# Kernel tuning notes

Hardware: AMD Instinct MI355X
Metric: run time of the kernel (lower is better)

## Reference

```python
import jax, jax.numpy as jnp
import numpy as np
from jax import lax

DG = 8  # deformable groups


def conv3(x, w, b):
    # 3x3 stride-1 SAME conv, NCHW/OIHW
    y = lax.conv_general_dilated(x, w, (1, 1), 'SAME',
                                 dimension_numbers=('NCHW', 'OIHW', 'NCHW'))
    return y + b[None, :, None, None]


def lrelu(x):
    return jnp.where(x >= 0, x, 0.1 * x)


def _mdcn(x, offset, mask, w, b, dg):
    """Modulated deformable conv v2: 3x3, stride 1, pad 1, dilation 1, groups 1.
    offset: [B, 2*dg*9, H, W] (first dg*9 = y offsets, second dg*9 = x offsets),
    mask:   [B, dg*9, H, W] (already sigmoided)."""
    B, C, H, W = x.shape
    kk = 9
    Cg = C // dg
    off = offset.reshape(B, 2, dg, kk, H, W)
    oy, ox = off[:, 0], off[:, 1]            # [B, dg, kk, H, W]
    m = mask.reshape(B, dg, kk, H, W)
    ky = (jnp.arange(kk) // 3 - 1).astype(x.dtype).reshape(1, 1, kk, 1, 1)
    kx = (jnp.arange(kk) % 3 - 1).astype(x.dtype).reshape(1, 1, kk, 1, 1)
    hg = jnp.arange(H, dtype=x.dtype).reshape(1, 1, 1, H, 1)
    wg = jnp.arange(W, dtype=x.dtype).reshape(1, 1, 1, 1, W)
    py = hg + ky + oy                        # sampling positions (pad=1 cancels k-1 shift)
    px = wg + kx + ox
    y0 = jnp.floor(py)
    x0 = jnp.floor(px)
    wy = py - y0
    wx = px - x0
    xg = x.reshape(B, dg, Cg, H * W)
    acc = jnp.zeros((B, dg, Cg, kk, H, W), x.dtype)
    for dy, dx, wgt in ((0.0, 0.0, (1 - wy) * (1 - wx)),
                        (0.0, 1.0, (1 - wy) * wx),
                        (1.0, 0.0, wy * (1 - wx)),
                        (1.0, 1.0, wy * wx)):
        yy = y0 + dy
        xx = x0 + dx
        valid = (yy >= 0) & (yy < H) & (xx >= 0) & (xx < W)
        yi = jnp.clip(yy, 0, H - 1).astype(jnp.int32)
        xi = jnp.clip(xx, 0, W - 1).astype(jnp.int32)
        idx = (yi * W + xi).reshape(B, dg, 1, kk * H * W)
        v = jnp.take_along_axis(xg, idx, axis=3).reshape(B, dg, Cg, kk, H, W)
        acc = acc + v * (wgt * valid.astype(x.dtype))[:, :, None]
    acc = acc * m[:, :, None]                # modulation mask
    sampled = acc.reshape(B, C, kk, H, W)
    out = jnp.einsum('bckhw,ock->bohw', sampled, w.reshape(w.shape[0], C, kk))
    return out + b[None, :, None, None]


def _dcn_pack(x, feat, w_om, b_om, w, b):
    out = conv3(feat, w_om, b_om)            # [B, 3*dg*9, H, W]
    o1, o2, mr = jnp.split(out, 3, axis=1)
    offset = jnp.concatenate([o1, o2], axis=1)
    mask = jax.nn.sigmoid(mr)
    return _mdcn(x, offset, mask, w, b, DG)


def _forward(ref, neb,
             w_oc1, b_oc1, w_om1, b_om1, w_dcn1, b_dcn1, w_fc, b_fc,
             w_cas1, b_cas1, w_cas2, b_cas2, w_om2, b_om2, w_dcn2, b_dcn2,
             w_ta1, b_ta1, w_ta2, b_ta2, w_ff, b_ff):
    start = ref
    # --- PCD alignment (nbr_feat_l = neb, ref_feat_l = ref) ---
    off = lrelu(conv3(jnp.concatenate([neb, ref], axis=1), w_oc1, b_oc1))
    feat = _dcn_pack(neb, off, w_om1, b_om1, w_dcn1, b_dcn1)
    feat = lrelu(conv3(feat, w_fc, b_fc))
    off = jnp.concatenate([feat, ref], axis=1)
    off = lrelu(conv3(lrelu(conv3(off, w_cas1, b_cas1)), w_cas2, b_cas2))
    feat = lrelu(_dcn_pack(feat, off, w_om2, b_om2, w_dcn2, b_dcn2))
    # --- TSA fusion (ref=ref, neb=feat) ---
    emb_ref = conv3(ref, w_ta1, b_ta1)
    emb = conv3(feat, w_ta2, b_ta2)
    corr = jnp.sum(emb * emb_ref, axis=1, keepdims=True)  # [B,1,H,W]
    feat = lrelu(conv3(ref * corr, w_ff, b_ff))
    return feat + start


def setup_inputs() -> dict:
    key = jax.random.key(0)
    ks = jax.random.split(key, 32)
    B, C, H, W = 4, 64, 180, 320
    s = 0.05
    p = lambda k, shape: (jax.random.normal(k, shape, jnp.float32) * s)
    OM = 3 * DG * 9  # 216
    return {
        'ref': jax.random.normal(ks[0], (B, C, H, W), jnp.float32),
        'neb': jax.random.normal(ks[1], (B, C, H, W), jnp.float32),
        'w_oc1': p(ks[2], (C, 2 * C, 3, 3)), 'b_oc1': p(ks[3], (C,)),
        'w_om1': p(ks[4], (OM, C, 3, 3)),    'b_om1': p(ks[5], (OM,)),
        'w_dcn1': p(ks[6], (C, C, 3, 3)),    'b_dcn1': p(ks[7], (C,)),
        'w_fc': p(ks[8], (C, C, 3, 3)),      'b_fc': p(ks[9], (C,)),
        'w_cas1': p(ks[10], (C, 2 * C, 3, 3)), 'b_cas1': p(ks[11], (C,)),
        'w_cas2': p(ks[12], (C, C, 3, 3)),   'b_cas2': p(ks[13], (C,)),
        'w_om2': p(ks[14], (OM, C, 3, 3)),   'b_om2': p(ks[15], (OM,)),
        'w_dcn2': p(ks[16], (C, C, 3, 3)),   'b_dcn2': p(ks[17], (C,)),
        'w_ta1': p(ks[18], (C, C, 3, 3)),    'b_ta1': p(ks[19], (C,)),
        'w_ta2': p(ks[20], (C, C, 3, 3)),    'b_ta2': p(ks[21], (C,)),
        'w_ff': p(ks[22], (C, C, 3, 3)),     'b_ff': p(ks[23], (C,)),
    }


def reference(ref, neb,
              w_oc1, b_oc1, w_om1, b_om1, w_dcn1, b_dcn1, w_fc, b_fc,
              w_cas1, b_cas1, w_cas2, b_cas2, w_om2, b_om2, w_dcn2, b_dcn2,
              w_ta1, b_ta1, w_ta2, b_ta2, w_ff, b_ff):
    return _forward(ref, neb,
                    w_oc1, b_oc1, w_om1, b_om1, w_dcn1, b_dcn1, w_fc, b_fc,
                    w_cas1, b_cas1, w_cas2, b_cas2, w_om2, b_om2, w_dcn2, b_dcn2,
                    w_ta1, b_ta1, w_ta2, b_ta2, w_ff, b_ff)
```

## Files before the change

### kernel.cpp

```cpp
#include <hip/hip_runtime.h>
#include <cmath>


using short8 = __attribute__((ext_vector_type(8))) short;
using f32x4  = __attribute__((ext_vector_type(4))) float;

#define DEVINL static __device__ __forceinline__

DEVINL unsigned short f2bf(float f){
    unsigned u = __float_as_uint(f);
    u += 0x7fffu + ((u >> 16) & 1u);
    return (unsigned short)(u >> 16);
}
DEVINL unsigned pack2(float a, float b){ return (unsigned)f2bf(a) | ((unsigned)f2bf(b) << 16); }
DEVINL float bflo(unsigned u){ return __uint_as_float(u << 16); }
DEVINL float bfhi(unsigned u){ return __uint_as_float(u & 0xffff0000u); }
DEVINL float bf2f(unsigned short u){ return __uint_as_float((unsigned)u << 16); }
DEVINL float lrelu_f(float v){ return v >= 0.f ? v : 0.1f * v; }

DEVINL void swz_decode(int& bx, int& by, int& bz){
    const int gx = gridDim.x, gy = gridDim.y;
    int lin = blockIdx.x + gx * (blockIdx.y + gy * blockIdx.z);
    int nwg = gx * gy * gridDim.z;
    int q = nwg >> 3, r = nwg & 7;
    int xcd = lin & 7, idx = lin >> 3;
    int swz = (xcd < r ? xcd * (q + 1) : r + xcd * q) + idx;
    bz = swz / (gx * gy);
    int rem = swz - bz * gx * gy;
    by = rem / gx; bx = rem - by * gx;
}

struct Ptr4 { unsigned short* p[4]; };

__global__ __launch_bounds__(256) void nchw2nhwc2(const float* __restrict__ inA,
                                                  const float* __restrict__ inB,
                                                  unsigned short* __restrict__ outA,
                                                  unsigned short* __restrict__ outB)
{
    constexpr int HW = 180 * 320;
    const int blk = blockIdx.x;
    const float* in = (blk < 900) ? inA : inB;
    unsigned short* out = (blk < 900) ? outA : outB;
    size_t idx = (size_t)(blk % 900) * 256 + threadIdx.x;
    size_t bb = idx / HW, p = idx % HW;
    const float* src = in + (bb * 64) * (size_t)HW + p;
    unsigned short* dst = out + idx * 64;
    #pragma unroll
    for (int c0 = 0; c0 < 64; c0 += 16) {
        unsigned r[8];
        #pragma unroll
        for (int q = 0; q < 8; ++q)
            r[q] = pack2(src[(size_t)(c0 + 2*q) * HW], src[(size_t)(c0 + 2*q + 1) * HW]);
        *(uint4*)(dst + c0)     = *(uint4*)&r[0];
        *(uint4*)(dst + c0 + 8) = *(uint4*)&r[4];
    }
}

struct PrepArgs {
    const float* src[11];
    unsigned short* dst[11];
    int cout[11]; int cin[11]; int nch[11]; int kind[11];
};

__global__ __launch_bounds__(256) void prep_all(PrepArgs a)
{
    const int t = blockIdx.y;
    const int idx = blockIdx.x * 256 + threadIdx.x;
    if (a.kind[t] == 1) {
        if (idx >= 36864) return;
        int kk = idx & 31, oc = (idx >> 5) & 63, s = idx >> 11;
        int k = s * 32 + kk;
        int gt = k >> 3, c8 = k & 7;
        int g = gt / 9, tp = gt - g * 9;
        a.dst[t][idx] = f2bf(a.src[t][((size_t)oc * 64 + g * 8 + c8) * 9 + tp]);
    } else {
        int cin = a.cin[t], cout = a.cout[t];
        int ncs = cin / 32;
        int total = a.nch[t] * 9 * ncs * 2048;
        if (idx >= total) return;
        int kk = idx & 31, oc_l = (idx >> 5) & 63, rest = idx >> 11;
        int cs = rest % ncs; int rest2 = rest / ncs;
        int j = rest2 % 9; int ch = rest2 / 9;
        int oc = ch * 64 + oc_l, c = cs * 32 + kk;
        float v = (oc < cout) ? a.src[t][((size_t)oc * cin + c) * 9 + j] : 0.f;
        a.dst[t][idx] = f2bf(v);
    }
}

template<int CIN, bool TWO_IN, bool ACT, bool SCALE, int OUTMODE, int NM, int NF>
__global__ __launch_bounds__(256, (CIN == 128 ? 2 : 3)) void conv_mfma(
    const unsigned short* __restrict__ in0, const unsigned short* __restrict__ in1,
    const unsigned short* __restrict__ wgt, const float* __restrict__ bias,
    unsigned short* __restrict__ out, const float* __restrict__ corr,
    const float* __restrict__ res, float* __restrict__ outf,
    Ptr4 omout, int choff, int zdiv, int COUT)
{
    constexpr int H = 180, W = 320, HW = H * W;
    constexpr int NCB = CIN / 8;
    constexpr int NCS = CIN / 32;
    constexpr int XW  = NF * 16 + 2;
    __shared__ __align__(16) unsigned char lds[6 * XW * CIN * 2];

    const int tid = threadIdx.x;
    int bx, by, bz;
    swz_decode(bx, by, bz);
    int b, ch;
    if (OUTMODE == 1) { b = bz / zdiv; ch = bz % zdiv + choff; }
    else              { b = bz; ch = 0; }
    const int x0 = bx * (NF * 16), y0 = by * 4;

    for (int t = tid; t < 6 * XW * NCB; t += 256) {
        int cb = t % NCB; int r = t / NCB;
        int xp = r % XW, yp = r / XW;
        int gx = x0 - 1 + xp, gy = y0 - 1 + yp;
        uint4 v = make_uint4(0, 0, 0, 0);
        if (gx >= 0 && gx < W && gy >= 0 && gy < H) {
            size_t pix = (size_t)b * HW + (size_t)gy * W + gx;
            const unsigned short* src;
            if (TWO_IN) src = (cb < 8) ? (in0 + pix * 64 + cb * 8) : (in1 + pix * 64 + (cb - 8) * 8);
            else        src = in0 + pix * CIN + cb * 8;
            v = *(const uint4*)src;
            if (SCALE) {
                float cv = corr[pix];
                v.x = pack2(bflo(v.x) * cv, bfhi(v.x) * cv);
                v.y = pack2(bflo(v.y) * cv, bfhi(v.y) * cv);
                v.z = pack2(bflo(v.z) * cv, bfhi(v.z) * cv);
                v.w = pack2(bflo(v.w) * cv, bfhi(v.w) * cv);
            }
        }
        int blk = cb ^ (xp & 7);
        *(uint4*)&lds[(size_t)((yp * XW + xp) * NCB + blk) * 16] = v;
    }
    __syncthreads();

    const int wv = tid >> 6, lane = tid & 63;
    const int ll = lane & 15, lh = lane >> 4;
    const unsigned short* wchunk = wgt + (size_t)ch * (9 * NCS * 2048);
    const int alane = ll * 32 + lh * 8;

    f32x4 acc[NM][NF];
    #pragma unroll
    for (int mi = 0; mi < NM; ++mi)
        #pragma unroll
        for (int nf = 0; nf < NF; ++nf) acc[mi][nf] = f32x4{0.f, 0.f, 0.f, 0.f};

    #pragma unroll
    for (int j = 0; j < 9; ++j) {
        const int jy = j / 3, jx = j % 3;
        #pragma unroll
        for (int cs = 0; cs < NCS; ++cs) {
            const int s = j * NCS + cs;
            short8 a[NM];
            #pragma unroll
            for (int mi = 0; mi < NM; ++mi)
                a[mi] = *(const short8*)(wchunk + (size_t)s * 2048 + mi * 512 + alane);
            short8 bf[NF];
            #pragma unroll
            for (int nf = 0; nf < NF; ++nf) {
                int xp = nf * 16 + ll + jx;
                int blk = (cs * 4 + lh) ^ (xp & 7);
                int addr = (((wv + jy) * XW + xp) * NCB + blk) * 16;
                bf[nf] = *(const short8*)&lds[addr];
            }
            #pragma unroll
            for (int mi = 0; mi < NM; ++mi)
                #pragma unroll
                for (int nf = 0; nf < NF; ++nf)
                    acc[mi][nf] = __builtin_amdgcn_mfma_f32_16x16x32_bf16(a[mi], bf[nf], acc[mi][nf], 0, 0, 0);
        }
    }

    const int py = y0 + wv;
    const size_t pixrow = (size_t)b * HW + (size_t)py * W;
    #pragma unroll
    for (int nf = 0; nf < NF; ++nf) {
        const int px = x0 + nf * 16 + ll;
        if (OUTMODE == 1) {
            unsigned short* oslot = omout.p[b];
            #pragma unroll
            for (int mi = 0; mi < NM; ++mi) {
                const int oc_l = mi * 16 + lh * 4;
                #pragma unroll
                for (int jj = 0; jj < 4; ++jj) {
                    int ocg = ch * 64 + oc_l + jj;
                    if (ocg < COUT) {
                        float t = acc[mi][nf][jj] + bias[ocg];
                        oslot[(size_t)ocg * HW + (size_t)py * W + px] = f2bf(ACT ? lrelu_f(t) : t);
                    }
                }
            }
        } else {
            #pragma unroll
            for (int mi = 0; mi < NM; ++mi) {
                const int oc_l = mi * 16 + lh * 4;
                if (OUTMODE == 0) {
                    float v[4];
                    #pragma unroll
                    for (int jj = 0; jj < 4; ++jj) {
                        float t = acc[mi][nf][jj] + bias[oc_l + jj];
                        v[jj] = ACT ? lrelu_f(t) : t;
                    }
                    uint2 st; st.x = pack2(v[0], v[1]); st.y = pack2(v[2], v[3]);
                    *(uint2*)&out[(pixrow + px) * 64 + oc_l] = st;
                } else {
                    #pragma unroll
                    for (int jj = 0; jj < 4; ++jj) {
                        int oc = oc_l + jj;
                        float t = acc[mi][nf][jj] + bias[oc];
                        if (ACT) t = lrelu_f(t);
                        size_t idx = ((size_t)b * 64 + oc) * HW + (size_t)py * W + px;
                        outf[idx] = t + res[idx];
                    }
                }
            }
        }
    }
}

__global__ __launch_bounds__(256, 3) void tacorr_mfma(
    const unsigned short* __restrict__ inR,
    const unsigned short* __restrict__ inE,
    const unsigned short* __restrict__ wR, const float* __restrict__ bR,
    const unsigned short* __restrict__ wE, const float* __restrict__ bE,
    float* __restrict__ outf)
{
    constexpr int H = 180, W = 320, HW = H * W;
    constexpr int NE1 = 6 * 34 * 8;
    __shared__ __align__(16) unsigned char lds[2][6 * 34 * 64 * 2];

    const int tid = threadIdx.x;
    int bx, by, bz;
    swz_decode(bx, by, bz);
    const int b = bz;
    const int x0 = bx * 32, y0 = by * 4;

    for (int t = tid; t < 2 * NE1; t += 256) {
        int half = t / NE1, e = t - half * NE1;
        int cb = e & 7; int r = e >> 3;
        int xp = r % 34, yp = r / 34;
        int gx = x0 - 1 + xp, gy = y0 - 1 + yp;
        uint4 v = make_uint4(0, 0, 0, 0);
        if (gx >= 0 && gx < W && gy >= 0 && gy < H) {
            size_t pix = (size_t)b * HW + (size_t)gy * W + gx;
            const unsigned short* src = (half ? inE : inR) + pix * 64 + cb * 8;
            v = *(const uint4*)src;
        }
        int blk = cb ^ (xp & 7);
        *(uint4*)&lds[half][(size_t)((yp * 34 + xp) * 8 + blk) * 16] = v;
    }
    __syncthreads();

    const int wv = tid >> 6, lane = tid & 63;
    const int ll = lane & 15, lh = lane >> 4;
    const int alane = ll * 32 + lh * 8;

    f32x4 accR[4][2], accE[4][2];
    #pragma unroll
    for (int mi = 0; mi < 4; ++mi)
        #pragma unroll
        for (int nf = 0; nf < 2; ++nf) { accR[mi][nf] = f32x4{0,0,0,0}; accE[mi][nf] = f32x4{0,0,0,0}; }

    #pragma unroll
    for (int j = 0; j < 9; ++j) {
        const int jy = j / 3, jx = j % 3;
        #pragma unroll
        for (int cs = 0; cs < 2; ++cs) {
            const int s = j * 2 + cs;
            short8 aR[4], aE[4];
            #pragma unroll
            for (int mi = 0; mi < 4; ++mi) {
                aR[mi] = *(const short8*)(wR + (size_t)s * 2048 + mi * 512 + alane);
                aE[mi] = *(const short8*)(wE + (size_t)s * 2048 + mi * 512 + alane);
            }
            #pragma unroll
            for (int nf = 0; nf < 2; ++nf) {
                int xp = nf * 16 + ll + jx;
                int blk = (cs * 4 + lh) ^ (xp & 7);
                int addr = (((wv + jy) * 34 + xp) * 8 + blk) * 16;
                short8 bfR = *(const short8*)&lds[0][addr];
                short8 bfE = *(const short8*)&lds[1][addr];
                #pragma unroll
                for (int mi = 0; mi < 4; ++mi) {
                    accR[mi][nf] = __builtin_amdgcn_mfma_f32_16x16x32_bf16(aR[mi], bfR, accR[mi][nf], 0, 0, 0);
                    accE[mi][nf] = __builtin_amdgcn_mfma_f32_16x16x32_bf16(aE[mi], bfE, accE[mi][nf], 0, 0, 0);
                }
            }
        }
    }

    const int py = y0 + wv;
    const size_t pixrow = (size_t)b * HW + (size_t)py * W;
    #pragma unroll
    for (int nf = 0; nf < 2; ++nf) {
        const int px = x0 + nf * 16 + ll;
        float dot = 0.f;
        #pragma unroll
        for (int mi = 0; mi < 4; ++mi) {
            const int oc_l = mi * 16 + lh * 4;
            #pragma unroll
            for (int jj = 0; jj < 4; ++jj)
                dot += (accR[mi][nf][jj] + bR[oc_l + jj]) * (accE[mi][nf][jj] + bE[oc_l + jj]);
        }
        dot += __shfl_xor(dot, 16);
        dot += __shfl_xor(dot, 32);
        if (lh == 0) outf[pixrow + px] = dot;
    }
}

template<int ACT>
__global__ __launch_bounds__(256, 4) void mdcn_mfma(
    const unsigned short* __restrict__ x, Ptr4 omslots,
    const unsigned short* __restrict__ wgt, const float* __restrict__ bias,
    unsigned short* __restrict__ out)
{
    constexpr int H = 180, W = 320, HW = H * W;
    constexpr size_t CHW = (size_t)HW * 64;
    __shared__ __align__(16) unsigned char sv[72 * 32 * 16];

    const int tid = threadIdx.x;
    int bx, by, bz;
    swz_decode(bx, by, bz);
    const unsigned short* xb  = x + (size_t)bz * CHW;
    const unsigned short* omb = omslots.p[bz];
    unsigned short* ob        = out + (size_t)bz * CHW;
    const int px0 = bx * 32;
    const int py  = by;

    {
        const int pxl = tid & 31, g = tid >> 5;
        const int px = px0 + pxl;
        const size_t p = (size_t)py * W + px;
        const unsigned short* omg = omb + (size_t)(g * 9) * HW + p;

        float oyv[9], oxv[9], mmv[9];
        #pragma unroll
        for (int k = 0; k < 9; ++k) oyv[k] = bf2f(omg[(size_t)k * HW]);
        #pragma unroll
        for (int k = 0; k < 9; ++k) oxv[k] = bf2f(omg[(size_t)(72 + k) * HW]);
        #pragma unroll
        for (int k = 0; k < 9; ++k) mmv[k] = bf2f(omg[(size_t)(144 + k) * HW]);

        #pragma unroll
        for (int k = 0; k < 9; ++k) {
            float m = 1.f / (1.f + __expf(-mmv[k]));
            float pyf = (float)(py + (k / 3) - 1) + oyv[k];
            float pxf = (float)(px + (k % 3) - 1) + oxv[k];
            float y0f = floorf(pyf), x0f = floorf(pxf);
            float wy = pyf - y0f, wx = pxf - x0f;
            int yi = (int)y0f, xi = (int)x0f;
            bool vy0 = (yi >= 0) && (yi < H);
            bool vy1 = (yi + 1 >= 0) && (yi + 1 < H);
            bool vx0 = (xi >= 0) && (xi < W);
            bool vx1 = (xi + 1 >= 0) && (xi + 1 < W);
            float w00 = (vy0 && vx0) ? (1.f - wy) * (1.f - wx) * m : 0.f;
            float w01 = (vy0 && vx1) ? (1.f - wy) * wx * m : 0.f;
            float w10 = (vy1 && vx0) ? wy * (1.f - wx) * m : 0.f;
            float w11 = (vy1 && vx1) ? wy * wx * m : 0.f;
            int yc0 = min(max(yi, 0), H - 1), yc1 = min(max(yi + 1, 0), H - 1);
            int xc0 = min(max(xi, 0), W - 1), xc1 = min(max(xi + 1, 0), W - 1);
            uint4 c00 = *(const uint4*)(xb + ((size_t)(yc0 * W + xc0) * 64 + g * 8));
            uint4 c01 = *(const uint4*)(xb + ((size_t)(yc0 * W + xc1) * 64 + g * 8));
            uint4 c10 = *(const uint4*)(xb + ((size_t)(yc1 * W + xc0) * 64 + g * 8));
            uint4 c11 = *(const uint4*)(xb + ((size_t)(yc1 * W + xc1) * 64 + g * 8));
            const unsigned* p00 = (const unsigned*)&c00;
            const unsigned* p01 = (const unsigned*)&c01;
            const unsigned* p10 = (const unsigned*)&c10;
            const unsigned* p11 = (const unsigned*)&c11;
            unsigned r[4];
            #pragma unroll
            for (int q = 0; q < 4; ++q) {
                float lo = w00 * bflo(p00[q]) + w01 * bflo(p01[q]) + w10 * bflo(p10[q]) + w11 * bflo(p11[q]);
                float hi = w00 * bfhi(p00[q]) + w01 * bfhi(p01[q]) + w10 * bfhi(p10[q]) + w11 * bfhi(p11[q]);
                r[q] = pack2(lo, hi);
            }
            *(uint4*)&sv[(size_t)((g * 9 + k) * 32 + pxl) * 16] = *(uint4*)r;
        }
    }
    __syncthreads();

    const int wv = tid >> 6, lane = tid & 63;
    const int ll = lane & 15, lh = lane >> 4;
    f32x4 acc[2] = {f32x4{0.f,0.f,0.f,0.f}, f32x4{0.f,0.f,0.f,0.f}};
    #pragma unroll
    for (int s = 0; s < 18; ++s) {
        short8 a = *(const short8*)(wgt + (size_t)(s * 64 + wv * 16 + ll) * 32 + lh * 8);
        #pragma unroll
        for (int nf = 0; nf < 2; ++nf) {
            short8 bb = *(const short8*)&sv[(size_t)s * 2048 + lh * 512 + (nf * 16 + ll) * 16];
            acc[nf] = __builtin_amdgcn_mfma_f32_16x16x32_bf16(a, bb, acc[nf], 0, 0, 0);
        }
    }
    #pragma unroll
    for (int nf = 0; nf < 2; ++nf) {
        int opx = px0 + nf * 16 + ll;
        int oc0 = wv * 16 + lh * 4;
        float v[4];
        #pragma unroll
        for (int jj = 0; jj < 4; ++jj) {
            float t = acc[nf][jj] + bias[oc0 + jj];
            v[jj] = ACT ? lrelu_f(t) : t;
        }
        uint2 st; st.x = pack2(v[0], v[1]); st.y = pack2(v[2], v[3]);
        *(uint2*)&ob[((size_t)py * W + opx) * 64 + oc0] = st;
    }
}

extern "C" void kernel_launch(void* const* d_in, const int* in_sizes, int n_in,
                              void* d_out, int out_size, void* d_ws, size_t ws_size,
                              hipStream_t stream)
{
    const float* ref    = (const float*)d_in[0];
    const float* neb    = (const float*)d_in[1];
    const float* w_oc1  = (const float*)d_in[2];  const float* b_oc1  = (const float*)d_in[3];
    const float* w_om1  = (const float*)d_in[4];  const float* b_om1  = (const float*)d_in[5];
    const float* w_dcn1 = (const float*)d_in[6];  const float* b_dcn1 = (const float*)d_in[7];
    const float* w_fc   = (const float*)d_in[8];  const float* b_fc   = (const float*)d_in[9];
    const float* w_cas1 = (const float*)d_in[10]; const float* b_cas1 = (const float*)d_in[11];
    const float* w_cas2 = (const float*)d_in[12]; const float* b_cas2 = (const float*)d_in[13];
    const float* w_om2  = (const float*)d_in[14]; const float* b_om2  = (const float*)d_in[15];
    const float* w_dcn2 = (const float*)d_in[16]; const float* b_dcn2 = (const float*)d_in[17];
    const float* w_ta1  = (const float*)d_in[18]; const float* b_ta1  = (const float*)d_in[19];
    const float* w_ta2  = (const float*)d_in[20]; const float* b_ta2  = (const float*)d_in[21];
    const float* w_ff   = (const float*)d_in[22]; const float* b_ff   = (const float*)d_in[23];

    constexpr int H = 180, W = 320, HW = H * W;
    constexpr size_t CHW = (size_t)HW * 64;
    constexpr size_t SLB = 4 * CHW * 2;
    constexpr size_t OMSLOT_EL = (size_t)HW * 216;
    constexpr size_t OMSLOT_B  = OMSLOT_EL * 2;

    char* wsb = (char*)d_ws;
    unsigned short* S0 = (unsigned short*)(wsb);
    unsigned short* S1 = (unsigned short*)(wsb + SLB);
    unsigned short* S2 = (unsigned short*)(wsb + 2 * SLB);
    unsigned short* S3 = (unsigned short*)(wsb + 3 * SLB);
    float* corrf = (float*)S3;
    unsigned short* ffw = (unsigned short*)(wsb + SLB + (2u << 20));

    char* doutb = (char*)d_out;
    unsigned short* omA0 = (unsigned short*)doutb;
    unsigned short* omA1 = omA0 + OMSLOT_EL;
    unsigned short* wb   = (unsigned short*)(doutb + 2 * OMSLOT_B);
    const bool big = ws_size >= 4 * SLB + 2 * OMSLOT_B;
    unsigned short* omB0 = (unsigned short*)(wsb + 4 * SLB);
    unsigned short* omB1 = omB0 + OMSLOT_EL;

    unsigned short* w_oc1p = wb + 0;
    unsigned short* w_om1p = wb + 73728;
    unsigned short* w_dcn1p= wb + 221184;
    unsigned short* w_fcp  = wb + 258048;
    unsigned short* w_cas1p= wb + 294912;
    unsigned short* w_cas2p= wb + 368640;
    unsigned short* w_om2p = wb + 405504;
    unsigned short* w_dcn2p= wb + 552960;
    unsigned short* w_ta1p = wb + 589824;
    unsigned short* w_ta2p = wb + 626688;
    unsigned short* w_ffp  = wb + 663552;

    dim3 blk(256);
    dim3 g4(10, 45, 4);
    dim3 g4w(5, 45, 4);
    Ptr4 none{};

    nchw2nhwc2<<<1800, blk, 0, stream>>>(ref, neb, S0, S1);

    {
        PrepArgs pa;
        const float* srcs[11] = {w_oc1, w_om1, w_dcn1, w_fc, w_cas1, w_cas2, w_om2, w_dcn2, w_ta1, w_ta2, w_ff};
        unsigned short* dsts[11] = {w_oc1p, w_om1p, w_dcn1p, w_fcp, w_cas1p, w_cas2p, w_om2p, w_dcn2p, w_ta1p, w_ta2p, w_ffp};
        int couts[11] = {64, 216, 0, 64, 64, 64, 216, 0, 64, 64, 64};
        int cins[11]  = {128, 64, 0, 64, 128, 64, 64, 0, 64, 64, 64};
        int nchs[11]  = {1, 4, 0, 1, 1, 1, 4, 0, 1, 1, 1};
        int kinds[11] = {0, 0, 1, 0, 0, 0, 0, 1, 0, 0, 0};
        for (int i = 0; i < 11; ++i) {
            pa.src[i] = srcs[i]; pa.dst[i] = dsts[i];
            pa.cout[i] = couts[i]; pa.cin[i] = cins[i]; pa.nch[i] = nchs[i]; pa.kind[i] = kinds[i];
        }
        prep_all<<<dim3(576, 11), blk, 0, stream>>>(pa);
    }

    conv_mfma<128, true, true, false, 0, 4, 2><<<g4, blk, 0, stream>>>(
        S1, S0, w_oc1p, b_oc1, S2, nullptr, nullptr, nullptr, none, 0, 1, 64);

    auto ompack = [&](const unsigned short* inp, const unsigned short* wp, const float* bp,
                      Ptr4 slots, int nb){
        conv_mfma<64, false, false, false, 1, 4, 4><<<dim3(5, 45, 3 * nb), blk, 0, stream>>>(
            inp, nullptr, wp, bp, nullptr, nullptr, nullptr, nullptr, slots, 0, 3, 216);
        conv_mfma<64, false, false, false, 1, 2, 4><<<dim3(5, 45, nb), blk, 0, stream>>>(
            inp, nullptr, wp, bp, nullptr, nullptr, nullptr, nullptr, slots, 3, 1, 216);
    };

    if (big) {
        Ptr4 slots{omA0, omA1, omB0, omB1};
        ompack(S2, w_om1p, b_om1, slots, 4);
        mdcn_mfma<0><<<dim3(10, 180, 4), blk, 0, stream>>>(S1, slots, w_dcn1p, b_dcn1, S3);
    } else {
        Ptr4 slots{omA0, omA1, nullptr, nullptr};
        for (int pp = 0; pp < 2; ++pp) {
            ompack(S2 + 2 * pp * CHW, w_om1p, b_om1, slots, 2);
            mdcn_mfma<0><<<dim3(10, 180, 2), blk, 0, stream>>>(S1 + 2 * pp * CHW, slots,
                                                               w_dcn1p, b_dcn1, S3 + 2 * pp * CHW);
        }
    }

    conv_mfma<64, false, true, false, 0, 4, 4><<<g4w, blk, 0, stream>>>(
        S3, nullptr, w_fcp, b_fc, S2, nullptr, nullptr, nullptr, none, 0, 1, 64);
    conv_mfma<128, true, true, false, 0, 4, 2><<<g4, blk, 0, stream>>>(
        S2, S0, w_cas1p, b_cas1, S1, nullptr, nullptr, nullptr, none, 0, 1, 64);
    conv_mfma<64, false, true, false, 0, 4, 4><<<g4w, blk, 0, stream>>>(
        S1, nullptr, w_cas2p, b_cas2, S3, nullptr, nullptr, nullptr, none, 0, 1, 64);

    if (big) {
        Ptr4 slots{omA0, omA1, omB0, omB1};
        ompack(S3, w_om2p, b_om2, slots, 4);
        mdcn_mfma<1><<<dim3(10, 180, 4), blk, 0, stream>>>(S2, slots, w_dcn2p, b_dcn2, S1);
    } else {
        Ptr4 slots{omA0, omA1, nullptr, nullptr};
        for (int pp = 0; pp < 2; ++pp) {
            ompack(S3 + 2 * pp * CHW, w_om2p, b_om2, slots, 2);
            mdcn_mfma<1><<<dim3(10, 180, 2), blk, 0, stream>>>(S2 + 2 * pp * CHW, slots,
                                                               w_dcn2p, b_dcn2, S1 + 2 * pp * CHW);
        }
    }

    tacorr_mfma<<<g4, blk, 0, stream>>>(S0, S1, w_ta1p, b_ta1, w_ta2p, b_ta2, corrf);

    hipMemcpyAsync(ffw, w_ffp, 36864 * 2, hipMemcpyDeviceToDevice, stream);

    conv_mfma<64, false, true, true, 2, 4, 4><<<g4w, blk, 0, stream>>>(
        S0, nullptr, ffw, b_ff, nullptr, corrf, ref, (float*)d_out, none, 0, 1, 64);
}
```

Baseline: 1.157 ms.

## Split deformable sampling into two phases to shrink LDS and raise occupancy

The modulated deformable conv kernel now samples taps 0-4 into shared memory, runs the first 10 MFMA k-steps, then reuses the buffer for taps 5-8 and the remaining 8 steps. The weight prep layout is reordered tap-major so each phase's K slices are contiguous. Shared memory drops from 72 to 40 rows and launch bounds rise from 4 to 6 blocks per CU, aiming to hide gather latency with more resident waves. Bilinear blending uses packed float2 math. The cost is two extra barriers per block and tighter register limits, which may cause spills.

After: 1.161 ms. About the same (+0.4%).

```diff
diff --git a/kernel.cpp b/kernel.cpp
--- a/kernel.cpp
+++ b/kernel.cpp
@@ -4,6 +4,7 @@
 
 using short8 = __attribute__((ext_vector_type(8))) short;
 using f32x4  = __attribute__((ext_vector_type(4))) float;
+using f32x2  = __attribute__((ext_vector_type(2))) float;
 
 #define DEVINL static __device__ __forceinline__
 
@@ -17,6 +18,9 @@
 DEVINL float bfhi(unsigned u){ return __uint_as_float(u & 0xffff0000u); }
 DEVINL float bf2f(unsigned short u){ return __uint_as_float((unsigned)u << 16); }
 DEVINL float lrelu_f(float v){ return v >= 0.f ? v : 0.1f * v; }
+DEVINL f32x2 up2(unsigned u){
+    return f32x2{__uint_as_float(u << 16), __uint_as_float(u & 0xffff0000u)};
+}
 
 DEVINL void swz_decode(int& bx, int& by, int& bz){
     const int gx = gridDim.x, gy = gridDim.y;
@@ -71,8 +75,8 @@
         int kk = idx & 31, oc = (idx >> 5) & 63, s = idx >> 11;
         int k = s * 32 + kk;
         int gt = k >> 3, c8 = k & 7;
-        int g = gt / 9, tp = gt - g * 9;
-        a.dst[t][idx] = f2bf(a.src[t][((size_t)oc * 64 + g * 8 + c8) * 9 + tp]);
+        int tap = gt >> 3, g = gt & 7;
+        a.dst[t][idx] = f2bf(a.src[t][((size_t)oc * 64 + g * 8 + c8) * 9 + tap]);
     } else {
         int cin = a.cin[t], cout = a.cout[t];
         int ncs = cin / 32;
@@ -308,14 +312,14 @@
 }
 
 template<int ACT>
-__global__ __launch_bounds__(256, 4) void mdcn_mfma(
+__global__ __launch_bounds__(256, 6) void mdcn_mfma(
     const unsigned short* __restrict__ x, Ptr4 omslots,
     const unsigned short* __restrict__ wgt, const float* __restrict__ bias,
     unsigned short* __restrict__ out)
 {
     constexpr int H = 180, W = 320, HW = H * W;
     constexpr size_t CHW = (size_t)HW * 64;
-    __shared__ __align__(16) unsigned char sv[72 * 32 * 16];
+    __shared__ __align__(16) unsigned char sv[40 * 32 * 16];
 
     const int tid = threadIdx.x;
     int bx, by, bz;
@@ -326,63 +330,63 @@
     const int px0 = bx * 32;
     const int py  = by;
 
-    {
-        const int pxl = tid & 31, g = tid >> 5;
-        const int px = px0 + pxl;
-        const size_t p = (size_t)py * W + px;
-        const unsigned short* omg = omb + (size_t)(g * 9) * HW + p;
-
-        float oyv[9], oxv[9], mmv[9];
-        #pragma unroll
-        for (int k = 0; k < 9; ++k) oyv[k] = bf2f(omg[(size_t)k * HW]);
-        #pragma unroll
-        for (int k = 0; k < 9; ++k) oxv[k] = bf2f(omg[(size_t)(72 + k) * HW]);
-        #pragma unroll
-        for (int k = 0; k < 9; ++k) mmv[k] = bf2f(omg[(size_t)(144 + k) * HW]);
-
-        #pragma unroll
-        for (int k = 0; k < 9; ++k) {
-            float m = 1.f / (1.f + __expf(-mmv[k]));
-            float pyf = (float)(py + (k / 3) - 1) + oyv[k];
-            float pxf = (float)(px + (k % 3) - 1) + oxv[k];
-            float y0f = floorf(pyf), x0f = floorf(pxf);
-            float wy = pyf - y0f, wx = pxf - x0f;
-            int yi = (int)y0f, xi = (int)x0f;
-            bool vy0 = (yi >= 0) && (yi < H);
-            bool vy1 = (yi + 1 >= 0) && (yi + 1 < H);
-            bool vx0 = (xi >= 0) && (xi < W);
-            bool vx1 = (xi + 1 >= 0) && (xi + 1 < W);
-            float w00 = (vy0 && vx0) ? (1.f - wy) * (1.f - wx) * m : 0.f;
-            float w01 = (vy0 && vx1) ? (1.f - wy) * wx * m : 0.f;
-            float w10 = (vy1 && vx0) ? wy * (1.f - wx) * m : 0.f;
-            float w11 = (vy1 && vx1) ? wy * wx * m : 0.f;
-            int yc0 = min(max(yi, 0), H - 1), yc1 = min(max(yi + 1, 0), H - 1);
-            int xc0 = min(max(xi, 0), W - 1), xc1 = min(max(xi + 1, 0), W - 1);
-            uint4 c00 = *(const uint4*)(xb + ((size_t)(yc0 * W + xc0) * 64 + g * 8));
-            uint4 c01 = *(const uint4*)(xb + ((size_t)(yc0 * W + xc1) * 64 + g * 8));
-            uint4 c10 = *(const uint4*)(xb + ((size_t)(yc1 * W + xc0) * 64 + g * 8));
-            uint4 c11 = *(const uint4*)(xb + ((size_t)(yc1 * W + xc1) * 64 + g * 8));
-            const unsigned* p00 = (const unsigned*)&c00;
-            const unsigned* p01 = (const unsigned*)&c01;
-            const unsigned* p10 = (const unsigned*)&c10;
-            const unsigned* p11 = (const unsigned*)&c11;
-            unsigned r[4];
-            #pragma unroll
-            for (int q = 0; q < 4; ++q) {
-                float lo = w00 * bflo(p00[q]) + w01 * bflo(p01[q]) + w10 * bflo(p10[q]) + w11 * bflo(p11[q]);
-                float hi = w00 * bfhi(p00[q]) + w01 * bfhi(p01[q]) + w10 * bfhi(p10[q]) + w11 * bfhi(p11[q]);
-                r[q] = pack2(lo, hi);
-            }
-            *(uint4*)&sv[(size_t)((g * 9 + k) * 32 + pxl) * 16] = *(uint4*)r;
-        }
-    }
-    __syncthreads();
+    const int pxl = tid & 31, g = tid >> 5;
+    const int px = px0 + pxl;
+    const size_t p = (size_t)py * W + px;
+    const unsigned short* omg = omb + (size_t)(g * 9) * HW + p;
+
+    float oyv[9], oxv[9], mmv[9];
+    #pragma unroll
+    for (int k = 0; k < 9; ++k) oyv[k] = bf2f(omg[(size_t)k * HW]);
+    #pragma unroll
+    for (int k = 0; k < 9; ++k) oxv[k] = bf2f(omg[(size_t)(72 + k) * HW]);
+    #pragma unroll
+    for (int k = 0; k < 9; ++k) mmv[k] = bf2f(omg[(size_t)(144 + k) * HW]);
+
+    auto SAMPLE = [&](int k, int row){
+        float m = 1.f / (1.f + __expf(-mmv[k]));
+        float pyf = (float)(py + (k / 3) - 1) + oyv[k];
+        float pxf = (float)(px + (k % 3) - 1) + oxv[k];
+        float y0f = floorf(pyf), x0f = floorf(pxf);
+        float wy = pyf - y0f, wx = pxf - x0f;
+        int yi = (int)y0f, xi = (int)x0f;
+        bool vy0 = (yi >= 0) && (yi < H);
+        bool vy1 = (yi + 1 >= 0) && (yi + 1 < H);
+        bool vx0 = (xi >= 0) && (xi < W);
+        bool vx1 = (xi + 1 >= 0) && (xi + 1 < W);
+        float w00 = (vy0 && vx0) ? (1.f - wy) * (1.f - wx) * m : 0.f;
+        float w01 = (vy0 && vx1) ? (1.f - wy) * wx * m : 0.f;
+        float w10 = (vy1 && vx0) ? wy * (1.f - wx) * m : 0.f;
+        float w11 = (vy1 && vx1) ? wy * wx * m : 0.f;
+        int yc0 = min(max(yi, 0), H - 1), yc1 = min(max(yi + 1, 0), H - 1);
+        int xc0 = min(max(xi, 0), W - 1), xc1 = min(max(xi + 1, 0), W - 1);
+        uint4 c00 = *(const uint4*)(xb + ((size_t)(yc0 * W + xc0) * 64 + g * 8));
+        uint4 c01 = *(const uint4*)(xb + ((size_t)(yc0 * W + xc1) * 64 + g * 8));
+        uint4 c10 = *(const uint4*)(xb + ((size_t)(yc1 * W + xc0) * 64 + g * 8));
+        uint4 c11 = *(const uint4*)(xb + ((size_t)(yc1 * W + xc1) * 64 + g * 8));
+        const unsigned* p00 = (const unsigned*)&c00;
+        const unsigned* p01 = (const unsigned*)&c01;
+        const unsigned* p10 = (const unsigned*)&c10;
+        const unsigned* p11 = (const unsigned*)&c11;
+        unsigned r[4];
+        #pragma unroll
+        for (int q = 0; q < 4; ++q) {
+            f32x2 rv = up2(p00[q]) * w00 + up2(p01[q]) * w01
+                     + up2(p10[q]) * w10 + up2(p11[q]) * w11;
+            r[q] = pack2(rv[0], rv[1]);
+        }
+        *(uint4*)&sv[(size_t)(row * 32 + pxl) * 16] = *(uint4*)r;
+    };
 
     const int wv = tid >> 6, lane = tid & 63;
     const int ll = lane & 15, lh = lane >> 4;
     f32x4 acc[2] = {f32x4{0.f,0.f,0.f,0.f}, f32x4{0.f,0.f,0.f,0.f}};
-    #pragma unroll
-    for (int s = 0; s < 18; ++s) {
+
+    #pragma unroll
+    for (int k = 0; k < 5; ++k) SAMPLE(k, k * 8 + g);
+    __syncthreads();
+    #pragma unroll
+    for (int s = 0; s < 10; ++s) {
         short8 a = *(const short8*)(wgt + (size_t)(s * 64 + wv * 16 + ll) * 32 + lh * 8);
         #pragma unroll
         for (int nf = 0; nf < 2; ++nf) {
@@ -390,6 +394,20 @@
             acc[nf] = __builtin_amdgcn_mfma_f32_16x16x32_bf16(a, bb, acc[nf], 0, 0, 0);
         }
     }
+    __syncthreads();
+    #pragma unroll
+    for (int k = 5; k < 9; ++k) SAMPLE(k, (k - 5) * 8 + g);
+    __syncthreads();
+    #pragma unroll
+    for (int s = 0; s < 8; ++s) {
+        short8 a = *(const short8*)(wgt + (size_t)((10 + s) * 64 + wv * 16 + ll) * 32 + lh * 8);
+        #pragma unroll
+        for (int nf = 0; nf < 2; ++nf) {
+            short8 bb = *(const short8*)&sv[(size_t)s * 2048 + lh * 512 + (nf * 16 + ll) * 16];
+            acc[nf] = __builtin_amdgcn_mfma_f32_16x16x32_bf16(a, bb, acc[nf], 0, 0, 0);
+        }
+    }
+
     #pragma unroll
     for (int nf = 0; nf < 2; ++nf) {
         int opx = px0 + nf * 16 + ll;
```

## Split 128-channel convs into two 64-channel LDS passes and stage offset-mask stores

Applied to the files above, without the earlier changes.

The conv kernel now always uses a 64-channel LDS tile and handles 128-channel inputs by looping over two halves, reloading the tile between them. This lets the two-input convs use the wider 64-pixel tile at three blocks per CU. The offset/mask output path first transposes results through LDS so the NCHW stores can be written as coalesced 16-byte vectors. The bilinear sampling in the deformable conv uses packed two-wide float math. The cost is an extra barrier and tile reload per half, and more shared-memory traffic in the output path.

After: 1.114 ms. -3.8%, faster.

```diff
diff --git a/kernel.cpp b/kernel.cpp
--- a/kernel.cpp
+++ b/kernel.cpp
@@ -4,6 +4,7 @@
 
 using short8 = __attribute__((ext_vector_type(8))) short;
 using f32x4  = __attribute__((ext_vector_type(4))) float;
+using f32x2  = __attribute__((ext_vector_type(2))) float;
 
 #define DEVINL static __device__ __forceinline__
 
@@ -17,6 +18,9 @@
 DEVINL float bfhi(unsigned u){ return __uint_as_float(u & 0xffff0000u); }
 DEVINL float bf2f(unsigned short u){ return __uint_as_float((unsigned)u << 16); }
 DEVINL float lrelu_f(float v){ return v >= 0.f ? v : 0.1f * v; }
+DEVINL f32x2 up2(unsigned u){
+    return f32x2{__uint_as_float(u << 16), __uint_as_float(u & 0xffff0000u)};
+}
 
 DEVINL void swz_decode(int& bx, int& by, int& bz){
     const int gx = gridDim.x, gy = gridDim.y;
@@ -87,19 +91,18 @@
     }
 }
 
-template<int CIN, bool TWO_IN, bool ACT, bool SCALE, int OUTMODE, int NM, int NF>
-__global__ __launch_bounds__(256, (CIN == 128 ? 2 : 3)) void conv_mfma(
+template<bool ACT, bool SCALE, int OUTMODE, int NM, int HALVES>
+__global__ __launch_bounds__(256, 3) void conv_mfma(
     const unsigned short* __restrict__ in0, const unsigned short* __restrict__ in1,
     const unsigned short* __restrict__ wgt, const float* __restrict__ bias,
     unsigned short* __restrict__ out, const float* __restrict__ corr,
     const float* __restrict__ res, float* __restrict__ outf,
-    Ptr4 omout, int choff, int zdiv, int COUT)
+    Ptr4 omout, int choff, int zdiv)
 {
     constexpr int H = 180, W = 320, HW = H * W;
-    constexpr int NCB = CIN / 8;
-    constexpr int NCS = CIN / 32;
-    constexpr int XW  = NF * 16 + 2;
-    __shared__ __align__(16) unsigned char lds[6 * XW * CIN * 2];
+    constexpr int NF = 4;
+    constexpr int XW = NF * 16 + 2;
+    __shared__ __align__(16) unsigned char lds[6 * XW * 64 * 2];
 
     const int tid = threadIdx.x;
     int bx, by, bz;
@@ -107,35 +110,11 @@
     int b, ch;
     if (OUTMODE == 1) { b = bz / zdiv; ch = bz % zdiv + choff; }
     else              { b = bz; ch = 0; }
-    const int x0 = bx * (NF * 16), y0 = by * 4;
-
-    for (int t = tid; t < 6 * XW * NCB; t += 256) {
-        int cb = t % NCB; int r = t / NCB;
-        int xp = r % XW, yp = r / XW;
-        int gx = x0 - 1 + xp, gy = y0 - 1 + yp;
-        uint4 v = make_uint4(0, 0, 0, 0);
-        if (gx >= 0 && gx < W && gy >= 0 && gy < H) {
-            size_t pix = (size_t)b * HW + (size_t)gy * W + gx;
-            const unsigned short* src;
-            if (TWO_IN) src = (cb < 8) ? (in0 + pix * 64 + cb * 8) : (in1 + pix * 64 + (cb - 8) * 8);
-            else        src = in0 + pix * CIN + cb * 8;
-            v = *(const uint4*)src;
-            if (SCALE) {
-                float cv = corr[pix];
-                v.x = pack2(bflo(v.x) * cv, bfhi(v.x) * cv);
-                v.y = pack2(bflo(v.y) * cv, bfhi(v.y) * cv);
-                v.z = pack2(bflo(v.z) * cv, bfhi(v.z) * cv);
-                v.w = pack2(bflo(v.w) * cv, bfhi(v.w) * cv);
-            }
-        }
-        int blk = cb ^ (xp & 7);
-        *(uint4*)&lds[(size_t)((yp * XW + xp) * NCB + blk) * 16] = v;
-    }
-    __syncthreads();
+    const int x0 = bx * 64, y0 = by * 4;
 
     const int wv = tid >> 6, lane = tid & 63;
     const int ll = lane & 15, lh = lane >> 4;
-    const unsigned short* wchunk = wgt + (size_t)ch * (9 * NCS * 2048);
+    const unsigned short* wchunk = wgt + (size_t)ch * (9 * 2 * 2048);
     const int alane = ll * 32 + lh * 8;
 
     f32x4 acc[NM][NF];
@@ -145,72 +124,117 @@
         for (int nf = 0; nf < NF; ++nf) acc[mi][nf] = f32x4{0.f, 0.f, 0.f, 0.f};
 
     #pragma unroll
-    for (int j = 0; j < 9; ++j) {
-        const int jy = j / 3, jx = j % 3;
-        #pragma unroll
-        for (int cs = 0; cs < NCS; ++cs) {
-            const int s = j * NCS + cs;
-            short8 a[NM];
+    for (int h = 0; h < HALVES; ++h) {
+        if (h) __syncthreads();
+        const unsigned short* srcb = (HALVES == 2 && h == 1) ? in1 : in0;
+        for (int t = tid; t < 6 * XW * 8; t += 256) {
+            int cb = t & 7; int r = t >> 3;
+            int xp = r % XW, yp = r / XW;
+            int gx = x0 - 1 + xp, gy = y0 - 1 + yp;
+            uint4 v = make_uint4(0, 0, 0, 0);
+            if (gx >= 0 && gx < W && gy >= 0 && gy < H) {
+                size_t pix = (size_t)b * HW + (size_t)gy * W + gx;
+                v = *(const uint4*)(srcb + pix * 64 + cb * 8);
+                if (SCALE) {
+                    float cv = corr[pix];
+                    v.x = pack2(bflo(v.x) * cv, bfhi(v.x) * cv);
+                    v.y = pack2(bflo(v.y) * cv, bfhi(v.y) * cv);
+                    v.z = pack2(bflo(v.z) * cv, bfhi(v.z) * cv);
+                    v.w = pack2(bflo(v.w) * cv, bfhi(v.w) * cv);
+                }
+            }
+            int blk = cb ^ (xp & 7);
+            *(uint4*)&lds[(size_t)((yp * XW + xp) * 8 + blk) * 16] = v;
+        }
+        __syncthreads();
+
+        #pragma unroll
+        for (int j = 0; j < 9; ++j) {
+            const int jy = j / 3, jx = j % 3;
             #pragma unroll
-            for (int mi = 0; mi < NM; ++mi)
-                a[mi] = *(const short8*)(wchunk + (size_t)s * 2048 + mi * 512 + alane);
-            short8 bf[NF];
-            #pragma unroll
-            for (int nf = 0; nf < NF; ++nf) {
-                int xp = nf * 16 + ll + jx;
-                int blk = (cs * 4 + lh) ^ (xp & 7);
-                int addr = (((wv + jy) * XW + xp) * NCB + blk) * 16;
-                bf[nf] = *(const short8*)&lds[addr];
-            }
-            #pragma unroll
-            for (int mi = 0; mi < NM; ++mi)
-                #pragma unroll
-                for (int nf = 0; nf < NF; ++nf)
-                    acc[mi][nf] = __builtin_amdgcn_mfma_f32_16x16x32_bf16(a[mi], bf[nf], acc[mi][nf], 0, 0, 0);
+            for (int csl = 0; csl < 2; ++csl) {
+                const int ws = j * (2 * HALVES) + h * 2 + csl;
+                short8 a[NM];
+                #pragma unroll
+                for (int mi = 0; mi < NM; ++mi)
+                    a[mi] = *(const short8*)(wchunk + (size_t)ws * 2048 + mi * 512 + alane);
+                short8 bf[NF];
+                #pragma unroll
+                for (int nf = 0; nf < NF; ++nf) {
+                    int xp = nf * 16 + ll + jx;
+                    int blk = (csl * 4 + lh) ^ (xp & 7);
+                    int addr = (((wv + jy) * XW + xp) * 8 + blk) * 16;
+                    bf[nf] = *(const short8*)&lds[addr];
+                }
+                #pragma unroll
+                for (int mi = 0; mi < NM; ++mi)
+                    #pragma unroll
+                    for (int nf = 0; nf < NF; ++nf)
+                        acc[mi][nf] = __builtin_amdgcn_mfma_f32_16x16x32_bf16(a[mi], bf[nf], acc[mi][nf], 0, 0, 0);
+            }
         }
     }
 
     const int py = y0 + wv;
     const size_t pixrow = (size_t)b * HW + (size_t)py * W;
+
+    if (OUTMODE == 1) {
+        __syncthreads();
+        unsigned short* t2 = (unsigned short*)lds;
+        #pragma unroll
+        for (int nf = 0; nf < NF; ++nf) {
+            const int px = nf * 16 + ll;
+            #pragma unroll
+            for (int mi = 0; mi < NM; ++mi) {
+                #pragma unroll
+                for (int jj = 0; jj < 4; ++jj) {
+                    int oc = mi * 16 + lh * 4 + jj;
+                    int ocg = ch * 64 + oc;
+                    if (ocg < 216) {
+                        float t = acc[mi][nf][jj] + bias[ocg];
+                        t2[(size_t)(wv * 64 + oc) * 72 + px] = f2bf(ACT ? lrelu_f(t) : t);
+                    }
+                }
+            }
+        }
+        __syncthreads();
+        unsigned short* oslot = omout.p[b];
+        #pragma unroll
+        for (int i = 0; i < 8; ++i) {
+            int gu = i * 32 + (tid >> 3), q = tid & 7;
+            int row = gu >> 6, oc = gu & 63;
+            int ocg = ch * 64 + oc;
+            if (oc < NM * 16 && ocg < 216) {
+                uint4 v = *(uint4*)&t2[(size_t)(row * 64 + oc) * 72 + q * 8];
+                *(uint4*)&oslot[(size_t)ocg * HW + (size_t)(y0 + row) * W + x0 + q * 8] = v;
+            }
+        }
+        return;
+    }
+
     #pragma unroll
     for (int nf = 0; nf < NF; ++nf) {
         const int px = x0 + nf * 16 + ll;
-        if (OUTMODE == 1) {
-            unsigned short* oslot = omout.p[b];
-            #pragma unroll
-            for (int mi = 0; mi < NM; ++mi) {
-                const int oc_l = mi * 16 + lh * 4;
+        #pragma unroll
+        for (int mi = 0; mi < NM; ++mi) {
+            const int oc_l = mi * 16 + lh * 4;
+            if (OUTMODE == 0) {
+                float v[4];
                 #pragma unroll
                 for (int jj = 0; jj < 4; ++jj) {
-                    int ocg = ch * 64 + oc_l + jj;
-                    if (ocg < COUT) {
-                        float t = acc[mi][nf][jj] + bias[ocg];
-                        oslot[(size_t)ocg * HW + (size_t)py * W + px] = f2bf(ACT ? lrelu_f(t) : t);
-                    }
+                    float t = acc[mi][nf][jj] + bias[oc_l + jj];
+                    v[jj] = ACT ? lrelu_f(t) : t;
                 }
-            }
-        } else {
-            #pragma unroll
-            for (int mi = 0; mi < NM; ++mi) {
-                const int oc_l = mi * 16 + lh * 4;
-                if (OUTMODE == 0) {
-                    float v[4];
-                    #pragma unroll
-                    for (int jj = 0; jj < 4; ++jj) {
-                        float t = acc[mi][nf][jj] + bias[oc_l + jj];
-                        v[jj] = ACT ? lrelu_f(t) : t;
-                    }
-                    uint2 st; st.x = pack2(v[0], v[1]); st.y = pack2(v[2], v[3]);
-                    *(uint2*)&out[(pixrow + px) * 64 + oc_l] = st;
-                } else {
-                    #pragma unroll
-                    for (int jj = 0; jj < 4; ++jj) {
-                        int oc = oc_l + jj;
-                        float t = acc[mi][nf][jj] + bias[oc];
-                        if (ACT) t = lrelu_f(t);
-                        size_t idx = ((size_t)b * 64 + oc) * HW + (size_t)py * W + px;
-                        outf[idx] = t + res[idx];
-                    }
+                uint2 st; st.x = pack2(v[0], v[1]); st.y = pack2(v[2], v[3]);
+                *(uint2*)&out[(pixrow + px) * 64 + oc_l] = st;
+            } else {
+                #pragma unroll
+                for (int jj = 0; jj < 4; ++jj) {
+                    int oc = oc_l + jj;
+                    float t = acc[mi][nf][jj] + bias[oc];
+                    if (ACT) t = lrelu_f(t);
+                    size_t idx = ((size_t)b * 64 + oc) * HW + (size_t)py * W + px;
+                    outf[idx] = t + res[idx];
                 }
             }
         }
@@ -369,9 +393,9 @@
             unsigned r[4];
             #pragma unroll
             for (int q = 0; q < 4; ++q) {
-                float lo = w00 * bflo(p00[q]) + w01 * bflo(p01[q]) + w10 * bflo(p10[q]) + w11 * bflo(p11[q]);
-                float hi = w00 * bfhi(p00[q]) + w01 * bfhi(p01[q]) + w10 * bfhi(p10[q]) + w11 * bfhi(p11[q]);
-                r[q] = pack2(lo, hi);
+                f32x2 rv = up2(p00[q]) * w00 + up2(p01[q]) * w01
+                         + up2(p10[q]) * w10 + up2(p11[q]) * w11;
+                r[q] = pack2(rv[0], rv[1]);
             }
             *(uint4*)&sv[(size_t)((g * 9 + k) * 32 + pxl) * 16] = *(uint4*)r;
         }
@@ -458,8 +482,8 @@
     unsigned short* w_ffp  = wb + 663552;
 
     dim3 blk(256);
-    dim3 g4(10, 45, 4);
-    dim3 g4w(5, 45, 4);
+    dim3 gw(5, 45, 4);
+    dim3 g2(10, 45, 4);
     Ptr4 none{};
 
     nchw2nhwc2<<<1800, blk, 0, stream>>>(ref, neb, S0, S1);
@@ -479,15 +503,15 @@
         prep_all<<<dim3(576, 11), blk, 0, stream>>>(pa);
     }
 
-    conv_mfma<128, true, true, false, 0, 4, 2><<<g4, blk, 0, stream>>>(
-        S1, S0, w_oc1p, b_oc1, S2, nullptr, nullptr, nullptr, none, 0, 1, 64);
+    conv_mfma<true, false, 0, 4, 2><<<gw, blk, 0, stream>>>(
+        S1, S0, w_oc1p, b_oc1, S2, nullptr, nullptr, nullptr, none, 0, 1);
 
     auto ompack = [&](const unsigned short* inp, const unsigned short* wp, const float* bp,
                       Ptr4 slots, int nb){
-        conv_mfma<64, false, false, false, 1, 4, 4><<<dim3(5, 45, 3 * nb), blk, 0, stream>>>(
-            inp, nullptr, wp, bp, nullptr, nullptr, nullptr, nullptr, slots, 0, 3, 216);
-        conv_mfma<64, false, false, false, 1, 2, 4><<<dim3(5, 45, nb), blk, 0, stream>>>(
-            inp, nullptr, wp, bp, nullptr, nullptr, nullptr, nullptr, slots, 3, 1, 216);
+        conv_mfma<false, false, 1, 4, 1><<<dim3(5, 45, 3 * nb), blk, 0, stream>>>(
+            inp, nullptr, wp, bp, nullptr, nullptr, nullptr, nullptr, slots, 0, 3);
+        conv_mfma<false, false, 1, 2, 1><<<dim3(5, 45, nb), blk, 0, stream>>>(
+            inp, nullptr, wp, bp, nullptr, nullptr, nullptr, nullptr, slots, 3, 1);
     };
 
     if (big) {
@@ -503,12 +527,12 @@
         }
     }
 
-    conv_mfma<64, false, true, false, 0, 4, 4><<<g4w, blk, 0, stream>>>(
-        S3, nullptr, w_fcp, b_fc, S2, nullptr, nullptr, nullptr, none, 0, 1, 64);
-    conv_mfma<128, true, true, false, 0, 4, 2><<<g4, blk, 0, stream>>>(
-        S2, S0, w_cas1p, b_cas1, S1, nullptr, nullptr, nullptr, none, 0, 1, 64);
-    conv_mfma<64, false, true, false, 0, 4, 4><<<g4w, blk, 0, stream>>>(
-        S1, nullptr, w_cas2p, b_cas2, S3, nullptr, nullptr, nullptr, none, 0, 1, 64);
+    conv_mfma<true, false, 0, 4, 1><<<gw, blk, 0, stream>>>(
+        S3, nullptr, w_fcp, b_fc, S2, nullptr, nullptr, nullptr, none, 0, 1);
+    conv_mfma<true, false, 0, 4, 2><<<gw, blk, 0, stream>>>(
+        S2, S0, w_cas1p, b_cas1, S1, nullptr, nullptr, nullptr, none, 0, 1);
+    conv_mfma<true, false, 0, 4, 1><<<gw, blk, 0, stream>>>(
+        S1, nullptr, w_cas2p, b_cas2, S3, nullptr, nullptr, nullptr, none, 0, 1);
 
     if (big) {
         Ptr4 slots{omA0, omA1, omB0, omB1};
@@ -523,10 +547,10 @@
         }
     }
 
-    tacorr_mfma<<<g4, blk, 0, stream>>>(S0, S1, w_ta1p, b_ta1, w_ta2p, b_ta2, corrf);
+    tacorr_mfma<<<g2, blk, 0, stream>>>(S0, S1, w_ta1p, b_ta1, w_ta2p, b_ta2, corrf);
 
     hipMemcpyAsync(ffw, w_ffp, 36864 * 2, hipMemcpyDeviceToDevice, stream);
 
-    conv_mfma<64, false, true, true, 2, 4, 4><<<g4w, blk, 0, stream>>>(
-        S0, nullptr, ffw, b_ff, nullptr, corrf, ref, (float*)d_out, none, 0, 1, 64);
-}
+    conv_mfma<true, true, 2, 4, 1><<<gw, blk, 0, stream>>>(
+        S0, nullptr, ffw, b_ff, nullptr, corrf, ref, (float*)d_out, none, 0, 1);
+}
```
